# Optimization experiments

Hardware: AMD Instinct MI355X
Metric: run time of the kernel (lower is better)

Reference implementation:

```python
import jax, jax.numpy as jnp
import numpy as np

ALPHA = 0.5
SMOOTHING = 0.1
_S = 0.7071
_DIRS = np.array([
    [0.0, 0.0, 1.0], [0.0, 0.0, -1.0], [0.0, -_S, _S], [0.0, -1.0, 0.0],
    [0.0, -_S, -_S], [0.0, _S, -_S], [0.0, 1.0, 0.0], [0.0, _S, _S],
    [_S, 0.0, _S], [1.0, 0.0, 0.0], [_S, 0.0, -_S], [-_S, 0.0, -_S],
    [-1.0, 0.0, 0.0], [-_S, 0.0, _S], [0.5, -_S, 0.5], [-0.5, -_S, -0.5],
    [-0.5, _S, -0.5], [0.5, _S, 0.5], [_S, -_S, 0.0], [-_S, -_S, 0.0],
    [-_S, _S, 0.0], [_S, _S, 0.0], [0.5, -_S, -0.5], [-0.5, -_S, 0.5],
    [-0.5, _S, 0.5], [0.5, _S, -0.5]], dtype=np.float32)

def _cosine_distance_matrix(d):
    # torch cosine_similarity with eps=1e-8: dot / (max(||a||,eps)*max(||b||,eps))
    n = np.maximum(np.linalg.norm(d, axis=1), 1e-8)  # [26]
    cos = (d @ d.T) / (n[:, None] * n[None, :])
    return (1.0 - cos).astype(np.float32)

LABEL_W = jnp.asarray(_cosine_distance_matrix(_DIRS))  # [26, 26]

def setup_inputs() -> dict:
    key = jax.random.key(0)
    k1, k2 = jax.random.split(key)
    B, C = 2000000, 26
    x = jax.random.normal(k1, (B, C), dtype=jnp.float32)
    target = jax.random.randint(k2, (B,), 0, C, dtype=jnp.int64)
    return {"x": x, "target": target}

def reference(x, target):
    n_class = x.shape[1]
    # --- direction-difference metric (non-differentiable argmax path) ---
    pred = jnp.argmax(x, axis=1)                     # [B]
    dir_diff = LABEL_W[pred, target] ** 2            # [B] fused 2D gather + pow
    dir_diff = dir_diff.mean()
    # --- label-smoothing cross entropy ---
    eps = SMOOTHING / n_class
    log_prb = jax.nn.log_softmax(x, axis=1)          # [B, C]
    one_hot = jax.nn.one_hot(target, n_class, dtype=x.dtype)
    one_hot = one_hot * (1.0 - eps) + (1.0 - one_hot) * (eps / (n_class - 1))
    ce = -(one_hot * log_prb).sum(axis=1).mean()
    return ALPHA * dir_diff + (1.0 - ALPHA) * ce
```

## Files before the change

### kernel.cpp

```cpp
#include <hip/hip_runtime.h>

#define BLOCK  256
#define ROWS   256
#define GRID   1280
#define NCLASS 26

__device__ __constant__ float c_dirs[26][3] = {
    {0.f,0.f,1.f},        {0.f,0.f,-1.f},       {0.f,-0.7071f,0.7071f}, {0.f,-1.f,0.f},
    {0.f,-0.7071f,-0.7071f},{0.f,0.7071f,-0.7071f},{0.f,1.f,0.f},        {0.f,0.7071f,0.7071f},
    {0.7071f,0.f,0.7071f},{1.f,0.f,0.f},        {0.7071f,0.f,-0.7071f},{-0.7071f,0.f,-0.7071f},
    {-1.f,0.f,0.f},       {-0.7071f,0.f,0.7071f},{0.5f,-0.7071f,0.5f},  {-0.5f,-0.7071f,-0.5f},
    {-0.5f,0.7071f,-0.5f},{0.5f,0.7071f,0.5f},  {0.7071f,-0.7071f,0.f},{-0.7071f,-0.7071f,0.f},
    {-0.7071f,0.7071f,0.f},{0.7071f,0.7071f,0.f},{0.5f,-0.7071f,-0.5f},{-0.5f,-0.7071f,0.5f},
    {-0.5f,0.7071f,0.5f}, {0.5f,0.7071f,-0.5f}};

__global__ __launch_bounds__(BLOCK) void cmdce_main(const float* __restrict__ x,
                                                    const int* __restrict__ tgt,
                                                    double* __restrict__ partial,
                                                    int B) {
    __shared__ float stage[ROWS * NCLASS];
    __shared__ float w2[26 * 26];
    __shared__ float wsum[BLOCK / 64];

    for (int idx = threadIdx.x; idx < 676; idx += BLOCK) {
        int p = idx / 26, t = idx - p * 26;
        float px = c_dirs[p][0], py = c_dirs[p][1], pz = c_dirs[p][2];
        float qx = c_dirs[t][0], qy = c_dirs[t][1], qz = c_dirs[t][2];
        float np_ = fmaxf(sqrtf(px*px + py*py + pz*pz), 1e-8f);
        float nq_ = fmaxf(sqrtf(qx*qx + qy*qy + qz*qz), 1e-8f);
        float cosv = (px*qx + py*qy + pz*qz) / (np_ * nq_);
        float w = 1.0f - cosv;
        w2[idx] = w * w;
    }

    int pairs = B >> 1;
    int pbase = pairs / GRID;
    int prem  = pairs % GRID;
    int b     = blockIdx.x;
    int p0    = b * pbase + min(b, prem);
    int np    = pbase + (b < prem ? 1 : 0);
    int r0    = p0 * 2;
    int nrows = np * 2;

    const float4* src = reinterpret_cast<const float4*>(x);
    float4* stage4 = reinterpret_cast<float4*>(stage);
    float acc = 0.0f;

    for (int off = 0; off < nrows; off += ROWS) {
        int rows_in = min(ROWS, nrows - off);
        int nvec = rows_in * NCLASS / 4;
        size_t vbase = (size_t)(r0 + off) * NCLASS / 4;
        __syncthreads();
        for (int i = threadIdx.x; i < nvec; i += BLOCK)
            stage4[i] = src[vbase + i];
        __syncthreads();

        if ((int)threadIdx.x < rows_in) {
            int r = r0 + off + threadIdx.x;
            float v[26];
            const float2* rowp = reinterpret_cast<const float2*>(&stage[threadIdx.x * NCLASS]);
            #pragma unroll
            for (int k = 0; k < 13; ++k) {
                float2 p = rowp[k];
                v[2 * k] = p.x;
                v[2 * k + 1] = p.y;
            }
            float m = v[0];
            int am = 0;
            #pragma unroll
            for (int j = 1; j < 26; ++j)
                if (v[j] > m) { m = v[j]; am = j; }
            float se = 0.0f, sx = 0.0f;
            #pragma unroll
            for (int j = 0; j < 26; ++j) {
                se += __expf(v[j] - m);
                sx += v[j];
            }
            int t = tgt[r];
            float xt = 0.0f;
            #pragma unroll
            for (int j = 0; j < 26; ++j) xt = (j == t) ? v[j] : xt;

            float ce = m + __logf(se) - (1.5384615384615385e-4f * sx + 0.996f * xt);
            acc += 0.5f * (w2[am * 26 + t] + ce);
        }
    }

    #pragma unroll
    for (int o = 32; o > 0; o >>= 1) acc += __shfl_down(acc, o);
    int lane = threadIdx.x & 63, wid = threadIdx.x >> 6;
    __syncthreads();
    if (lane == 0) wsum[wid] = acc;
    __syncthreads();
    if (threadIdx.x == 0) {
        float s = 0.0f;
        #pragma unroll
        for (int w = 0; w < BLOCK / 64; ++w) s += wsum[w];
        partial[b] = (double)s;
    }
}

__global__ __launch_bounds__(BLOCK) void cmdce_final(const double* __restrict__ partial,
                                                     float* __restrict__ out, int B, int n) {
    __shared__ double wsum[BLOCK / 64];
    double a = 0.0;
    for (int i = threadIdx.x; i < n; i += BLOCK) a += partial[i];
    #pragma unroll
    for (int off = 32; off > 0; off >>= 1) a += __shfl_down(a, off);
    int lane = threadIdx.x & 63, wid = threadIdx.x >> 6;
    if (lane == 0) wsum[wid] = a;
    __syncthreads();
    if (threadIdx.x == 0) {
        double s = 0.0;
        #pragma unroll
        for (int w = 0; w < BLOCK / 64; ++w) s += wsum[w];
        out[0] = (float)(s / (double)B);
    }
}

extern "C" void kernel_launch(void* const* d_in, const int* in_sizes, int n_in,
                              void* d_out, int out_size, void* d_ws, size_t ws_size,
                              hipStream_t stream) {
    const float* x   = (const float*)d_in[0];
    const int*   tgt = (const int*)d_in[1];
    float*  out = (float*)d_out;
    double* partial = (double*)d_ws;
    int B = in_sizes[1];

    cmdce_main<<<GRID, BLOCK, 0, stream>>>(x, tgt, partial, B);
    cmdce_final<<<1, BLOCK, 0, stream>>>(partial, out, B, GRID);
}
```

Measured before the change: 41.37 us.

## Prefetch next chunk into registers while computing current chunk

```diff
diff --git a/kernel.cpp b/kernel.cpp
--- a/kernel.cpp
+++ b/kernel.cpp
@@ -4,6 +4,7 @@
 #define ROWS   256
 #define GRID   1280
 #define NCLASS 26
+#define NVREG  7
 
 __device__ __constant__ float c_dirs[26][3] = {
     {0.f,0.f,1.f},        {0.f,0.f,-1.f},       {0.f,-0.7071f,0.7071f}, {0.f,-1.f,0.f},
@@ -44,21 +45,48 @@
 
     const float4* src = reinterpret_cast<const float4*>(x);
     float4* stage4 = reinterpret_cast<float4*>(stage);
+    const int tid = threadIdx.x;
     float acc = 0.0f;
 
-    for (int off = 0; off < nrows; off += ROWS) {
+    int nchunks = (nrows + ROWS - 1) / ROWS;
+    float4 regs[NVREG];
+
+    int nvec_cur = min(ROWS, nrows) * NCLASS / 4;
+    {
+        size_t vb = (size_t)r0 * NCLASS / 4;
+        #pragma unroll
+        for (int k = 0; k < NVREG; ++k) {
+            int i = tid + k * BLOCK;
+            if (i < nvec_cur) regs[k] = src[vb + i];
+        }
+    }
+
+    for (int c = 0; c < nchunks; ++c) {
+        int off = c * ROWS;
         int rows_in = min(ROWS, nrows - off);
-        int nvec = rows_in * NCLASS / 4;
-        size_t vbase = (size_t)(r0 + off) * NCLASS / 4;
+
         __syncthreads();
-        for (int i = threadIdx.x; i < nvec; i += BLOCK)
-            stage4[i] = src[vbase + i];
+        #pragma unroll
+        for (int k = 0; k < NVREG; ++k) {
+            int i = tid + k * BLOCK;
+            if (i < nvec_cur) stage4[i] = regs[k];
+        }
+        if (c + 1 < nchunks) {
+            int rows2 = min(ROWS, nrows - (off + ROWS));
+            nvec_cur = rows2 * NCLASS / 4;
+            size_t vb = (size_t)(r0 + off + ROWS) * NCLASS / 4;
+            #pragma unroll
+            for (int k = 0; k < NVREG; ++k) {
+                int i = tid + k * BLOCK;
+                if (i < nvec_cur) regs[k] = src[vb + i];
+            }
+        }
         __syncthreads();
 
-        if ((int)threadIdx.x < rows_in) {
-            int r = r0 + off + threadIdx.x;
+        if (tid < rows_in) {
+            int r = r0 + off + tid;
             float v[26];
-            const float2* rowp = reinterpret_cast<const float2*>(&stage[threadIdx.x * NCLASS]);
+            const float2* rowp = reinterpret_cast<const float2*>(&stage[tid * NCLASS]);
             #pragma unroll
             for (int k = 0; k < 13; ++k) {
                 float2 p = rowp[k];
```

Result: slower. 117.0 us (+182.9%).
